# Optimization experiments

Hardware: AMD Instinct MI355X
Metric: run time of the kernel (lower is better)

Reference implementation:

```python
import jax, jax.numpy as jnp
import numpy as np

LN_EPS = 1e-5

def _ln(x, w, b):
    mu = jnp.mean(x, -1, keepdims=True)
    var = jnp.mean((x - mu) ** 2, -1, keepdims=True)
    return (x - mu) / jnp.sqrt(var + LN_EPS) * w + b

def _rot_fwd(x, c, s):
    dh = x.shape[-1] // 2
    r, i = x[..., :dh], x[..., dh:]
    return jnp.concatenate([r * c - i * s, r * s + i * c], axis=-1)

def _rot_inv(x, c, s):
    dh = x.shape[-1] // 2
    r, i = x[..., :dh], x[..., dh:]
    return jnp.concatenate([r * c + i * s, -r * s + i * c], axis=-1)

def _sheaf(x, thetas, alpha, corr_W):
    # causal offsets for window=3
    B, T, d = x.shape
    offsets = [-3, -2, -1, 0]
    lap = jnp.zeros_like(x)
    for idx, delta in enumerate(offsets):
        th = thetas[idx]
        c, s = jnp.cos(th), jnp.sin(th)
        Rx = _rot_fwd(x, c, s)
        if delta == 0:
            x_nb = x
        else:
            ad = -delta
            zeros = jnp.zeros((B, ad, d), dtype=x.dtype)
            x_nb = jnp.concatenate([zeros, x[:, :T - ad, :]], axis=1)
        lap = lap + _rot_inv(Rx - x_nb, c, s)
    out = x - jnp.abs(alpha) * lap
    return out + jnp.einsum('btd,od->bto', out, corr_W)

def _gist_rotation(x, gist_theta, gist_mag, gist_weights, gist_strength, ln_w, ln_b):
    # Scale-1 path: gist_weights present. theta: (B, dh)
    dh = x.shape[-1] // 2
    w = gist_weights[..., None] * gist_mag              # (B, K, 1)
    w = w / (jnp.sum(w, axis=1, keepdims=True) + 1e-8)
    theta = jnp.sum(w * gist_theta, axis=1)             # (B, dh)
    theta = theta * jax.nn.sigmoid(gist_strength)
    c = jnp.cos(theta)[:, None, :]                      # (B, 1, dh)
    s = jnp.sin(theta)[:, None, :]
    r, i = x[..., :dh], x[..., dh:]
    rot = jnp.concatenate([r * c - i * s, r * s + i * c], axis=-1)
    return _ln(rot, ln_w, ln_b)

def _gist_cross_attn(x, gist_theta, gist_mag, Wq, Wk, Wv, Wo, gist_up_W, gist_up_b, n_heads=16):
    B, T, d = x.shape
    K = gist_theta.shape[1]
    dh = d // n_heads
    gist_repr = jnp.einsum('bkf,of->bko', jnp.concatenate([gist_theta, gist_mag], axis=-1), gist_up_W) + gist_up_b  # (B,K,d)
    Q = jnp.einsum('btd,od->bto', x, Wq).reshape(B, T, n_heads, dh).transpose(0, 2, 1, 3)          # (B,H,T,dh)
    Kh = jnp.einsum('bkd,od->bko', gist_repr, Wk).reshape(B, K, n_heads, dh).transpose(0, 2, 1, 3)  # (B,H,K,dh)
    V = jnp.einsum('bkd,od->bko', gist_repr, Wv).reshape(B, K, n_heads, dh).transpose(0, 2, 1, 3)
    scores = jnp.einsum('bhtd,bhkd->bhtk', Q, Kh) / jnp.sqrt(jnp.asarray(dh, x.dtype))
    ctx = jnp.einsum('bhtk,bhkd->bhtd', jax.nn.softmax(scores, axis=-1), V)
    ctx = ctx.transpose(0, 2, 1, 3).reshape(B, T, d)
    return jnp.einsum('btd,od->bto', ctx, Wo)

def _forward(x, gist_theta, gist_mag, gist_weights,
             ln_sheaf_w, ln_sheaf_b, sheaf_thetas, alpha, corr_W,
             ln_gist_w, ln_gist_b, gist_strength, gr_ln_w, gr_ln_b,
             ln_gca_w, ln_gca_b, Wq, Wk, Wv, Wo, gist_up_W, gist_up_b):
    x = x + _sheaf(_ln(x, ln_sheaf_w, ln_sheaf_b), sheaf_thetas, alpha, corr_W)
    xn = _ln(x, ln_gist_w, ln_gist_b)
    x = x + (_gist_rotation(xn, gist_theta, gist_mag, gist_weights, gist_strength, gr_ln_w, gr_ln_b) - xn)
    x = x + _gist_cross_attn(_ln(x, ln_gca_w, ln_gca_b), gist_theta, gist_mag,
                             Wq, Wk, Wv, Wo, gist_up_W, gist_up_b)
    return x

def setup_inputs() -> dict:
    key = jax.random.key(0)
    ks = jax.random.split(key, 16)
    B, T, d, K = 4, 2048, 2048, 16
    dh = d // 2
    scale = 1.0 / np.sqrt(d)
    inp = {
        'x': jax.random.normal(ks[0], (B, T, d), jnp.float32),
        'gist_theta': jax.random.normal(ks[1], (B, K, dh), jnp.float32),
        'gist_mag': jax.random.uniform(ks[2], (B, K, 1), jnp.float32),
        'gist_weights': jax.random.uniform(ks[3], (B, K), jnp.float32),
        'ln_sheaf_w': jnp.ones((d,), jnp.float32),
        'ln_sheaf_b': jnp.zeros((d,), jnp.float32),
        'sheaf_thetas': 0.1 * jax.random.normal(ks[4], (4, dh), jnp.float32),
        'alpha': jnp.asarray(0.15, jnp.float32),
        'corr_W': scale * jax.random.normal(ks[5], (d, d), jnp.float32),
        'ln_gist_w': jnp.ones((d,), jnp.float32),
        'ln_gist_b': jnp.zeros((d,), jnp.float32),
        'gist_strength': jnp.asarray(0.0, jnp.float32),
        'gr_ln_w': jnp.ones((d,), jnp.float32),
        'gr_ln_b': jnp.zeros((d,), jnp.float32),
        'ln_gca_w': jnp.ones((d,), jnp.float32),
        'ln_gca_b': jnp.zeros((d,), jnp.float32),
        'Wq': scale * jax.random.normal(ks[6], (d, d), jnp.float32),
        'Wk': scale * jax.random.normal(ks[7], (d, d), jnp.float32),
        'Wv': scale * jax.random.normal(ks[8], (d, d), jnp.float32),
        'Wo': scale * jax.random.normal(ks[9], (d, d), jnp.float32),
        'gist_up_W': (1.0 / np.sqrt(dh + 1)) * jax.random.normal(ks[10], (d, dh + 1), jnp.float32),
        'gist_up_b': jnp.zeros((d,), jnp.float32),
    }
    return inp

def reference(x, gist_theta, gist_mag, gist_weights,
              ln_sheaf_w, ln_sheaf_b, sheaf_thetas, alpha, corr_W,
              ln_gist_w, ln_gist_b, gist_strength, gr_ln_w, gr_ln_b,
              ln_gca_w, ln_gca_b, Wq, Wk, Wv, Wo, gist_up_W, gist_up_b):
    return _forward(x, gist_theta, gist_mag, gist_weights,
                    ln_sheaf_w, ln_sheaf_b, sheaf_thetas, alpha, corr_W,
                    ln_gist_w, ln_gist_b, gist_strength, gr_ln_w, gr_ln_b,
                    ln_gca_w, ln_gca_b, Wq, Wk, Wv, Wo, gist_up_W, gist_up_b)
```

## Files before the change

kernel.cpp:

```cpp
#include <hip/hip_runtime.h>
#include <hip/hip_bf16.h>

typedef unsigned short u16;
typedef unsigned int   u32;

using frag_ab = __attribute__((ext_vector_type(8))) short;
using frag_cd = __attribute__((ext_vector_type(4))) float;

__device__ __forceinline__ float bf2f(u16 u) {
    union { u32 i; float f; } v; v.i = ((u32)u) << 16; return v.f;
}
__device__ __forceinline__ u16 f2bf(float f) {
    __hip_bfloat16 h = __float2bfloat16(f);
    u16 u; __builtin_memcpy(&u, &h, 2); return u;
}
__device__ __forceinline__ float lo2f(u32 u) { union { u32 i; float f; } v; v.i = u << 16; return v.f; }
__device__ __forceinline__ float hi2f(u32 u) { union { u32 i; float f; } v; v.i = u & 0xffff0000u; return v.f; }
__device__ __forceinline__ void unpack8(uint4 v, float* f) {
    f[0]=lo2f(v.x); f[1]=hi2f(v.x); f[2]=lo2f(v.y); f[3]=hi2f(v.y);
    f[4]=lo2f(v.z); f[5]=hi2f(v.z); f[6]=lo2f(v.w); f[7]=hi2f(v.w);
}
__device__ __forceinline__ void load4f(const u16* p, float* f) {
    ushort4 v = *reinterpret_cast<const ushort4*>(p);
    f[0]=bf2f(v.x); f[1]=bf2f(v.y); f[2]=bf2f(v.z); f[3]=bf2f(v.w);
}
__device__ __forceinline__ void store4bf(u16* p, const float* f) {
    ushort4 v; v.x=f2bf(f[0]); v.y=f2bf(f[1]); v.z=f2bf(f[2]); v.w=f2bf(f[3]);
    *reinterpret_cast<ushort4*>(p) = v;
}
__device__ __forceinline__ u32 pack2(float a, float b) {
    return (u32)f2bf(a) | ((u32)f2bf(b) << 16);
}

__device__ __forceinline__ void gld16(const u16* g, u16* l) {
    __builtin_amdgcn_global_load_lds(
        (const __attribute__((address_space(1))) u32*)g,
        (__attribute__((address_space(3))) u32*)l, 16, 0, 0);
}

__device__ __forceinline__ void block_reduce2(float& s, float& ss, float* red) {
    #pragma unroll
    for (int off = 32; off > 0; off >>= 1) {
        s  += __shfl_down(s, off, 64);
        ss += __shfl_down(ss, off, 64);
    }
    int wv = threadIdx.x >> 6, ln = threadIdx.x & 63;
    if (ln == 0) { red[wv*2] = s; red[wv*2+1] = ss; }
    __syncthreads();
    s  = red[0] + red[2] + red[4] + red[6];
    ss = red[1] + red[3] + red[5] + red[7];
    __syncthreads();
}

__global__ __launch_bounds__(256) void convert_kernel(
    const float* __restrict__ in, u16* __restrict__ out, int n4)
{
    int i = blockIdx.x * 256 + threadIdx.x;
    if (i < n4) {
        float4 v = reinterpret_cast<const float4*>(in)[i];
        ushort4 o; o.x=f2bf(v.x); o.y=f2bf(v.y); o.z=f2bf(v.z); o.w=f2bf(v.w);
        reinterpret_cast<ushort4*>(out)[i] = o;
    }
}

__global__ __launch_bounds__(256) void apad_kernel(
    const float* __restrict__ gth, const float* __restrict__ gmag,
    u16* __restrict__ Abuf)
{
    const int r = blockIdx.x;
    const int tid = threadIdx.x;
    for (int c0 = tid*4; c0 < 1056; c0 += 1024) {
        float f[4];
        #pragma unroll
        for (int i = 0; i < 4; ++i) {
            int c = c0 + i;
            f[i] = (c < 1024) ? gth[(size_t)r*1024 + c] : (c == 1024 ? gmag[r] : 0.f);
        }
        store4bf(Abuf + (size_t)r*1056 + c0, f);
    }
}

__global__ __launch_bounds__(256) void wpad_kernel(
    const float* __restrict__ upW, u16* __restrict__ Bbuf)
{
    const int r = blockIdx.x;
    const int tid = threadIdx.x;
    for (int c0 = tid*4; c0 < 1056; c0 += 1024) {
        float f[4];
        #pragma unroll
        for (int i = 0; i < 4; ++i) {
            int c = c0 + i;
            f[i] = (c < 1025) ? upW[(size_t)r*1025 + c] : 0.f;
        }
        store4bf(Bbuf + (size_t)r*1056 + c0, f);
    }
}

__global__ __launch_bounds__(256) void setup_kernel(
    const float* __restrict__ sheaf_th, const float* __restrict__ gth,
    const float* __restrict__ gmag, const float* __restrict__ gwts,
    const float* __restrict__ strength, float* __restrict__ sheaf_cs,
    float* __restrict__ gist_cs)
{
    int bx = blockIdx.x, tid = threadIdx.x;
    if (bx < 4) {
        for (int j = tid; j < 1024; j += 256) {
            float th = sheaf_th[bx*1024 + j];
            sheaf_cs[bx*1024 + j]        = cosf(th);
            sheaf_cs[4096 + bx*1024 + j] = sinf(th);
        }
    } else {
        int b = bx - 4;
        float w[16], wsum = 0.f;
        #pragma unroll
        for (int k = 0; k < 16; ++k) {
            w[k] = gwts[b*16+k] * gmag[b*16+k];
            wsum += w[k];
        }
        float inv = 1.f / (wsum + 1e-8f);
        float sig = 1.f / (1.f + expf(-strength[0]));
        for (int j = tid; j < 1024; j += 256) {
            float th = 0.f;
            #pragma unroll
            for (int k = 0; k < 16; ++k)
                th += w[k] * inv * gth[(size_t)(b*16+k)*1024 + j];
            th *= sig;
            gist_cs[b*1024 + j]        = cosf(th);
            gist_cs[4096 + b*1024 + j] = sinf(th);
        }
    }
}

__global__ __launch_bounds__(256) void ln_kernel(
    const float* __restrict__ in, const float* __restrict__ w,
    const float* __restrict__ b, u16* __restrict__ out)
{
    __shared__ float red[8];
    const size_t base = (size_t)blockIdx.x * 2048;
    const int e0 = threadIdx.x * 8;
    float x[8];
    *reinterpret_cast<float4*>(&x[0]) = *reinterpret_cast<const float4*>(in + base + e0);
    *reinterpret_cast<float4*>(&x[4]) = *reinterpret_cast<const float4*>(in + base + e0 + 4);
    float s = 0.f, ss = 0.f;
    #pragma unroll
    for (int i = 0; i < 8; ++i) { s += x[i]; ss += x[i]*x[i]; }
    block_reduce2(s, ss, red);
    const float mu = s * (1.f/2048.f);
    const float rin = rsqrtf(ss * (1.f/2048.f) - mu*mu + 1e-5f);
    float wv[8], bv[8];
    *reinterpret_cast<float4*>(&wv[0]) = *reinterpret_cast<const float4*>(w + e0);
    *reinterpret_cast<float4*>(&wv[4]) = *reinterpret_cast<const float4*>(w + e0 + 4);
    *reinterpret_cast<float4*>(&bv[0]) = *reinterpret_cast<const float4*>(b + e0);
    *reinterpret_cast<float4*>(&bv[4]) = *reinterpret_cast<const float4*>(b + e0 + 4);
    float o[8];
    #pragma unroll
    for (int i = 0; i < 8; ++i) o[i] = (x[i]-mu)*rin*wv[i] + bv[i];
    uint4 st = { pack2(o[0],o[1]), pack2(o[2],o[3]), pack2(o[4],o[5]), pack2(o[6],o[7]) };
    *reinterpret_cast<uint4*>(out + base + e0) = st;
}

__global__ __launch_bounds__(256) void sheaf_kernel(
    const u16* __restrict__ x1, const float* __restrict__ scs,
    const float* __restrict__ alpha_p, u16* __restrict__ pre)
{
    const int row = blockIdx.x;
    const int t = row & 2047;
    const int j0 = threadIdx.x * 4;
    const size_t base = (size_t)row * 2048;
    const float a = fabsf(alpha_p[0]);

    float xr[4], xi[4];
    load4f(x1 + base + j0, xr);
    load4f(x1 + base + 1024 + j0, xi);
    float lr[4], li[4];
    #pragma unroll
    for (int m = 0; m < 4; ++m) { lr[m] = 4.f*xr[m]; li[m] = 4.f*xi[m]; }

    #pragma unroll
    for (int idx = 0; idx < 4; ++idx) {
        const int sh = 3 - idx;
        if (t >= sh) {
            const float4 c4 = *reinterpret_cast<const float4*>(&scs[idx*1024 + j0]);
            const float4 s4 = *reinterpret_cast<const float4*>(&scs[4096 + idx*1024 + j0]);
            float c[4] = {c4.x, c4.y, c4.z, c4.w};
            float sn[4] = {s4.x, s4.y, s4.z, s4.w};
            float yr[4], yi[4];
            load4f(x1 + base - (size_t)sh*2048 + j0, yr);
            load4f(x1 + base - (size_t)sh*2048 + 1024 + j0, yi);
            #pragma unroll
            for (int m = 0; m < 4; ++m) {
                lr[m] -= yr[m]*c[m] + yi[m]*sn[m];
                li[m] -= yi[m]*c[m] - yr[m]*sn[m];
            }
        }
    }
    float pr[4], pi[4];
    #pragma unroll
    for (int m = 0; m < 4; ++m) { pr[m] = xr[m] - a*lr[m]; pi[m] = xi[m] - a*li[m]; }
    store4bf(pre + base + j0, pr);
    store4bf(pre + base + 1024 + j0, pi);
}

__global__ __launch_bounds__(256) void stage2_kernel(
    const u16* __restrict__ xA, const float* __restrict__ gcs,
    const float* __restrict__ lgw, const float* __restrict__ lgb,
    const float* __restrict__ grw, const float* __restrict__ grb,
    const float* __restrict__ gcaw, const float* __restrict__ gcab,
    u16* __restrict__ xB, u16* __restrict__ x2)
{
    __shared__ float red[8];
    const int row = blockIdx.x;
    const int b = row >> 11;
    const int j0 = threadIdx.x * 4;
    const size_t base = (size_t)row * 2048;

    float ar[4], ai[4];
    load4f(xA + base + j0, ar);
    load4f(xA + base + 1024 + j0, ai);

    float s = 0.f, ss = 0.f;
    #pragma unroll
    for (int m = 0; m < 4; ++m) { s += ar[m]+ai[m]; ss += ar[m]*ar[m] + ai[m]*ai[m]; }
    block_reduce2(s, ss, red);
    float mu = s * (1.f/2048.f);
    float rin = rsqrtf(ss * (1.f/2048.f) - mu*mu + 1e-5f);

    float w0[4], b0[4], w1[4], b1[4];
    *reinterpret_cast<float4*>(w0) = *reinterpret_cast<const float4*>(lgw + j0);
    *reinterpret_cast<float4*>(b0) = *reinterpret_cast<const float4*>(lgb + j0);
    *reinterpret_cast<float4*>(w1) = *reinterpret_cast<const float4*>(lgw + 1024 + j0);
    *reinterpret_cast<float4*>(b1) = *reinterpret_cast<const float4*>(lgb + 1024 + j0);
    float xnr[4], xni[4];
    #pragma unroll
    for (int m = 0; m < 4; ++m) {
        xnr[m] = (ar[m]-mu)*rin*w0[m] + b0[m];
        xni[m] = (ai[m]-mu)*rin*w1[m] + b1[m];
    }

    const float4 c4 = *reinterpret_cast<const float4*>(&gcs[b*1024 + j0]);
    const float4 s4 = *reinterpret_cast<const float4*>(&gcs[4096 + b*1024 + j0]);
    float c[4] = {c4.x, c4.y, c4.z, c4.w};
    float sn[4] = {s4.x, s4.y, s4.z, s4.w};
    float rr[4], ri[4];
    #pragma unroll
    for (int m = 0; m < 4; ++m) {
        rr[m] = xnr[m]*c[m] - xni[m]*sn[m];
        ri[m] = xnr[m]*sn[m] + xni[m]*c[m];
    }

    s = 0.f; ss = 0.f;
    #pragma unroll
    for (int m = 0; m < 4; ++m) { s += rr[m]+ri[m]; ss += rr[m]*rr[m] + ri[m]*ri[m]; }
    block_reduce2(s, ss, red);
    float mu2 = s * (1.f/2048.f);
    float rin2 = rsqrtf(ss * (1.f/2048.f) - mu2*mu2 + 1e-5f);

    *reinterpret_cast<float4*>(w0) = *reinterpret_cast<const float4*>(grw + j0);
    *reinterpret_cast<float4*>(b0) = *reinterpret_cast<const float4*>(grb + j0);
    *reinterpret_cast<float4*>(w1) = *reinterpret_cast<const float4*>(grw + 1024 + j0);
    *reinterpret_cast<float4*>(b1) = *reinterpret_cast<const float4*>(grb + 1024 + j0);
    float br[4], bi[4];
    #pragma unroll
    for (int m = 0; m < 4; ++m) {
        float gr_ = (rr[m]-mu2)*rin2*w0[m] + b0[m];
        float gi_ = (ri[m]-mu2)*rin2*w1[m] + b1[m];
        br[m] = ar[m] - xnr[m] + gr_;
        bi[m] = ai[m] - xni[m] + gi_;
    }
    store4bf(xB + base + j0, br);
    store4bf(xB + base + 1024 + j0, bi);

    s = 0.f; ss = 0.f;
    #pragma unroll
    for (int m = 0; m < 4; ++m) { s += br[m]+bi[m]; ss += br[m]*br[m] + bi[m]*bi[m]; }
    block_reduce2(s, ss, red);
    float mu3 = s * (1.f/2048.f);
    float rin3 = rsqrtf(ss * (1.f/2048.f) - mu3*mu3 + 1e-5f);

    *reinterpret_cast<float4*>(w0) = *reinterpret_cast<const float4*>(gcaw + j0);
    *reinterpret_cast<float4*>(b0) = *reinterpret_cast<const float4*>(gcab + j0);
    *reinterpret_cast<float4*>(w1) = *reinterpret_cast<const float4*>(gcaw + 1024 + j0);
    *reinterpret_cast<float4*>(b1) = *reinterpret_cast<const float4*>(gcab + 1024 + j0);
    float o0[4], o1[4];
    #pragma unroll
    for (int m = 0; m < 4; ++m) {
        o0[m] = (br[m]-mu3)*rin3*w0[m] + b0[m];
        o1[m] = (bi[m]-mu3)*rin3*w1[m] + b1[m];
    }
    store4bf(x2 + base + j0, o0);
    store4bf(x2 + base + 1024 + j0, o1);
}

__global__ __launch_bounds__(256) void attn_kernel(
    const u16* __restrict__ Q, const u16* __restrict__ KV,
    u16* __restrict__ ctx)
{
    const int wv = threadIdx.x >> 6;
    const int lane = threadIdx.x & 63;
    const int tg = blockIdx.x * 4 + wv;
    const int b = tg >> 11;
    const size_t base = (size_t)tg * 2048 + lane * 32;

    float q[32];
    #pragma unroll
    for (int c = 0; c < 4; ++c)
        unpack8(*reinterpret_cast<const uint4*>(Q + base + c*8), &q[c*8]);

    float sc[16];
    #pragma unroll
    for (int k = 0; k < 16; ++k) {
        const u16* kr = KV + (size_t)(b*16 + k) * 4096 + lane*32;
        float p = 0.f;
        #pragma unroll
        for (int c = 0; c < 4; ++c) {
            float kv8[8]; unpack8(*reinterpret_cast<const uint4*>(kr + c*8), kv8);
            #pragma unroll
            for (int e = 0; e < 8; ++e) p += q[c*8+e] * kv8[e];
        }
        sc[k] = p;
    }
    #pragma unroll
    for (int k = 0; k < 16; ++k) {
        sc[k] += __shfl_xor(sc[k], 1, 64);
        sc[k] += __shfl_xor(sc[k], 2, 64);
        sc[k] *= 0.08838834764831845f;
    }
    float m = sc[0];
    #pragma unroll
    for (int k = 1; k < 16; ++k) m = fmaxf(m, sc[k]);
    float sum = 0.f;
    #pragma unroll
    for (int k = 0; k < 16; ++k) { sc[k] = expf(sc[k]-m); sum += sc[k]; }
    const float inv = 1.f / sum;

    float o[32];
    #pragma unroll
    for (int e = 0; e < 32; ++e) o[e] = 0.f;
    #pragma unroll
    for (int k = 0; k < 16; ++k) {
        const float p = sc[k] * inv;
        const u16* vr = KV + (size_t)(b*16 + k) * 4096 + 2048 + lane*32;
        #pragma unroll
        for (int c = 0; c < 4; ++c) {
            float v8[8]; unpack8(*reinterpret_cast<const uint4*>(vr + c*8), v8);
            #pragma unroll
            for (int e = 0; e < 8; ++e) o[c*8+e] += p * v8[e];
        }
    }
    #pragma unroll
    for (int c = 0; c < 4; ++c) {
        uint4 st = { pack2(o[c*8+0],o[c*8+1]), pack2(o[c*8+2],o[c*8+3]),
                     pack2(o[c*8+4],o[c*8+5]), pack2(o[c*8+6],o[c*8+7]) };
        *reinterpret_cast<uint4*>(ctx + base + c*8) = st;
    }
}

#define BM 128
#define BN 128
#define BK 32

template<int OUTF32>
__global__ __launch_bounds__(256) void gemm_bt_kernel(
    const u16* __restrict__ A, const u16* __restrict__ B,
    void* __restrict__ Cv, const float* __restrict__ addf,
    const u16* __restrict__ addb, const float* __restrict__ biasN,
    int M, int N, int K)
{
    __shared__ u16 As[2][8*512];
    __shared__ u16 Bs[2][8*512];

    const int tid = threadIdx.x;
    const int lane = tid & 63;
    const int wave = tid >> 6;
    const int wm = wave >> 1;
    const int wn = wave & 1;
    const int row0 = blockIdx.y * BM;
    const int col0 = blockIdx.x * BN;

    frag_cd acc[4][4] = {};

    const int srow   = lane >> 2;
    const int schunk = (lane & 3) ^ ((lane >> 3) & 3);
    const int scol   = schunk * 8;
    const int s0 = wave, s1 = wave + 4;

    int ra0 = row0 + s0*16 + srow; if (ra0 >= M) ra0 = M - 1;
    int ra1 = row0 + s1*16 + srow; if (ra1 >= M) ra1 = M - 1;
    const u16* gA0 = A + (size_t)ra0 * K + scol;
    const u16* gA1 = A + (size_t)ra1 * K + scol;
    const u16* gB0 = B + (size_t)(col0 + s0*16 + srow) * K + scol;
    const u16* gB1 = B + (size_t)(col0 + s1*16 + srow) * K + scol;

    const int fr = lane & 15;
    const int fq8 = lane >> 4;
    const int fslot = (4*fr + (fq8 ^ ((fr >> 1) & 3))) * 8;

    const int nt = K / BK;

    gld16(gA0, &As[0][s0*512]);
    gld16(gA1, &As[0][s1*512]);
    gld16(gB0, &Bs[0][s0*512]);
    gld16(gB1, &Bs[0][s1*512]);
    __syncthreads();

    int cur = 0;
    for (int t = 0; t < nt; ++t) {
        if (t + 1 < nt) {
            const int kt = (t + 1) * BK;
            gld16(gA0 + kt, &As[cur^1][s0*512]);
            gld16(gA1 + kt, &As[cur^1][s1*512]);
            gld16(gB0 + kt, &Bs[cur^1][s0*512]);
            gld16(gB1 + kt, &Bs[cur^1][s1*512]);
        }

        frag_ab af[4], bf_[4];
        #pragma unroll
        for (int i = 0; i < 4; ++i)
            af[i] = *reinterpret_cast<const frag_ab*>(&As[cur][(wm*4 + i)*512 + fslot]);
        #pragma unroll
        for (int j = 0; j < 4; ++j)
            bf_[j] = *reinterpret_cast<const frag_ab*>(&Bs[cur][(wn*4 + j)*512 + fslot]);
        #pragma unroll
        for (int i = 0; i < 4; ++i)
            #pragma unroll
            for (int j = 0; j < 4; ++j)
                acc[i][j] = __builtin_amdgcn_mfma_f32_16x16x32_bf16(af[i], bf_[j], acc[i][j], 0, 0, 0);

        __syncthreads();
        cur ^= 1;
    }

    #pragma unroll
    for (int i = 0; i < 4; ++i) {
        #pragma unroll
        for (int j = 0; j < 4; ++j) {
            #pragma unroll
            for (int r = 0; r < 4; ++r) {
                const int grow = row0 + wm*64 + i*16 + (lane >> 4) * 4 + r;
                const int gcol = col0 + wn*64 + j*16 + (lane & 15);
                if (grow < M) {
                    const size_t idx = (size_t)grow * N + gcol;
                    float v = acc[i][j][r];
                    if (addf) v += addf[idx];
                    if (addb) v += bf2f(addb[idx]);
                    if (biasN) v += biasN[gcol];
                    if (OUTF32) reinterpret_cast<float*>(Cv)[idx] = v;
                    else        reinterpret_cast<u16*>(Cv)[idx] = f2bf(v);
                }
            }
        }
    }
}

template<int OUTF32>
__global__ __launch_bounds__(512, 2) void gemm256_kernel(
    const u16* __restrict__ A, const u16* __restrict__ B,
    void* __restrict__ Cv, const float* __restrict__ addf,
    const u16* __restrict__ addb, const float* __restrict__ biasN,
    int M, int N, int K)
{
    extern __shared__ u16 lds[];
    u16* Abase = lds;
    u16* Bbase = lds + 32768;

    const int tid  = threadIdx.x;
    const int lane = tid & 63;
    const int wave = tid >> 6;
    const int wm   = wave >> 2;
    const int wn   = wave & 3;
    const int row0 = blockIdx.y * 256;
    const int col0 = blockIdx.x * 256;

    const int srow = lane >> 2;
    const int scol = ((lane & 3) ^ ((lane >> 3) & 3)) * 8;

    const u16* pA = A + (size_t)(row0 + wave*16 + srow) * K + scol;
    const u16* pB = B + (size_t)(col0 + wave*16 + srow) * K + scol;
    const size_t h128 = (size_t)128 * K;

    const int ldsW = wave * 1024;

    const int fr = lane & 15;
    const int fq8 = lane >> 4;
    const int fslot = (4*fr + (fq8 ^ ((fr >> 1) & 3))) * 8;

    frag_cd acc[8][4] = {};
    frag_ab bfr[4][2];
    frag_ab afr[2][2][2];

#define STAGE256(SRC, DSTOFF, KT)                                   \
    gld16((SRC) + (KT),      (DSTOFF) + ldsW);                      \
    gld16((SRC) + (KT) + 32, (DSTOFF) + ldsW + 512);

    STAGE256(pB,        Bbase + 0*8192, 0);
    STAGE256(pB + h128, Bbase + 1*8192, 0);
    STAGE256(pA,        Abase + 0*8192, 0);
    STAGE256(pA + h128, Abase + 1*8192, 0);
    STAGE256(pB,        Bbase + 2*8192, 64);
    STAGE256(pB + h128, Bbase + 3*8192, 64);
    asm volatile("s_waitcnt vmcnt(4)" ::: "memory");
    __builtin_amdgcn_s_barrier();
    {
        const u16* Ah = Abase + (0*2 + wm)*8192;
        #pragma unroll
        for (int r = 0; r < 2; ++r)
            #pragma unroll
            for (int ks = 0; ks < 2; ++ks)
                afr[0][r][ks] = *reinterpret_cast<const frag_ab*>(
                    Ah + ((r)*2*1 + (2*0 + r)*0 + ((0 + r)*2 + ks)*512 - (r)*2 + fslot));
    }

    const int NI = K >> 7;
    for (int i = 0; i < NI; ++i) {
        const int t1k = i*128 + 64;
        int t2k = i*128 + 128; if (t2k >= K) t2k = K - 64;
        int t3k = i*128 + 192; if (t3k >= K) t3k = K - 64;

        #pragma unroll
        for (int p = 0; p < 8; ++p) {
            const int q = p & 3;
            const int bufc = p >> 2;

            if (q == 0) {
                const u16* Bh = Bbase + (bufc*2 + (wn >> 1))*8192;
                #pragma unroll
                for (int n = 0; n < 4; ++n)
                    #pragma unroll
                    for (int ks = 0; ks < 2; ++ks)
                        bfr[n][ks] = *reinterpret_cast<const frag_ab*>(
                            Bh + (((wn & 1)*4 + n)*2 + ks)*512 + fslot);
            }
            switch (p) {
                case 0: STAGE256(pA,        Abase + 2*8192, t1k); break;
                case 1: STAGE256(pA + h128, Abase + 3*8192, t1k); break;
                case 2: STAGE256(pB,        Bbase + 0*8192, t2k); break;
                case 3: STAGE256(pB + h128, Bbase + 1*8192, t2k); break;
                case 4: STAGE256(pA,        Abase + 0*8192, t2k); break;
                case 5: STAGE256(pA + h128, Abase + 1*8192, t2k); break;
                case 6: STAGE256(pB,        Bbase + 2*8192, t3k); break;
                case 7: STAGE256(pB + h128, Bbase + 3*8192, t3k); break;
            }
            if (q == 3) asm volatile("s_waitcnt vmcnt(4)" ::: "memory");
            __builtin_amdgcn_s_barrier();
            asm volatile("s_waitcnt lgkmcnt(0)" ::: "memory");
            __builtin_amdgcn_sched_barrier(0);

            {
                const int qn = (q + 1) & 3;
                const int bufn = (q == 3) ? (bufc ^ 1) : bufc;
                const u16* Ah = Abase + (bufn*2 + wm)*8192;
                #pragma unroll
                for (int r = 0; r < 2; ++r)
                    #pragma unroll
                    for (int ks = 0; ks < 2; ++ks)
                        afr[(p+1)&1][r][ks] = *reinterpret_cast<const frag_ab*>(
                            Ah + ((2*qn + r)*2 + ks)*512 + fslot);
            }

            __builtin_amdgcn_s_setprio(1);
            #pragma unroll
            for (int ks = 0; ks < 2; ++ks)
                #pragma unroll
                for (int r = 0; r < 2; ++r)
                    #pragma unroll
                    for (int n = 0; n < 4; ++n)
                        acc[2*q + r][n] = __builtin_amdgcn_mfma_f32_16x16x32_bf16(
                            afr[p&1][r][ks], bfr[n][ks], acc[2*q + r][n], 0, 0, 0);
            __builtin_amdgcn_s_setprio(0);
            __builtin_amdgcn_s_barrier();
        }
    }
    asm volatile("s_waitcnt vmcnt(0)" ::: "memory");
#undef STAGE256

    #pragma unroll
    for (int m = 0; m < 8; ++m) {
        #pragma unroll
        for (int n = 0; n < 4; ++n) {
            #pragma unroll
            for (int r = 0; r < 4; ++r) {
                const int grow = row0 + wm*128 + m*16 + (lane >> 4) * 4 + r;
                const int gcol = col0 + wn*64 + n*16 + (lane & 15);
                {
                    const size_t idx = (size_t)grow * N + gcol;
                    float v = acc[m][n][r];
                    if (addf) v += addf[idx];
                    if (addb) v += bf2f(addb[idx]);
                    if (biasN) v += biasN[gcol];
                    if (OUTF32) reinterpret_cast<float*>(Cv)[idx] = v;
                    else        reinterpret_cast<u16*>(Cv)[idx] = f2bf(v);
                }
            }
        }
    }
}

extern "C" void kernel_launch(void* const* d_in, const int* in_sizes, int n_in,
                              void* d_out, int out_size, void* d_ws, size_t ws_size,
                              hipStream_t stream)
{
    const float* x          = (const float*)d_in[0];
    const float* gist_theta = (const float*)d_in[1];
    const float* gist_mag   = (const float*)d_in[2];
    const float* gist_wts   = (const float*)d_in[3];
    const float* ln_sheaf_w = (const float*)d_in[4];
    const float* ln_sheaf_b = (const float*)d_in[5];
    const float* sheaf_th   = (const float*)d_in[6];
    const float* alpha      = (const float*)d_in[7];
    const float* corr_W     = (const float*)d_in[8];
    const float* ln_gist_w  = (const float*)d_in[9];
    const float* ln_gist_b  = (const float*)d_in[10];
    const float* strength   = (const float*)d_in[11];
    const float* gr_w       = (const float*)d_in[12];
    const float* gr_b       = (const float*)d_in[13];
    const float* gca_w      = (const float*)d_in[14];
    const float* gca_b      = (const float*)d_in[15];
    const float* Wq         = (const float*)d_in[16];
    const float* Wk         = (const float*)d_in[17];
    const float* Wv         = (const float*)d_in[18];
    const float* Wo         = (const float*)d_in[19];
    const float* up_W       = (const float*)d_in[20];
    const float* up_b       = (const float*)d_in[21];
    float* out = (float*)d_out;

    static bool attr_done = false;
    if (!attr_done) {
        hipFuncSetAttribute((const void*)&gemm256_kernel<0>,
                            hipFuncAttributeMaxDynamicSharedMemorySize, 131072);
        hipFuncSetAttribute((const void*)&gemm256_kernel<1>,
                            hipFuncAttributeMaxDynamicSharedMemorySize, 131072);
        attr_done = true;
    }

    char* w = (char*)d_ws;
    const size_t BIG = (size_t)4 * 2048 * 2048 * sizeof(u16);
    u16* wA = (u16*)(w);
    u16* wB = (u16*)(w + BIG);
    u16* wC = (u16*)(w + 2*BIG);
    u16* wslot = (u16*)(w + 3*BIG);
    char* small = w + 3*BIG + (size_t)2048*2048*sizeof(u16);
    float* sheaf_cs = (float*)(small);
    float* gist_cs  = (float*)(small + 32768);
    u16* repr = (u16*)(small + 65536);
    u16* KV   = repr + 64*2048;

    const int W4 = 2048*2048/4;
    const dim3 gBig256(2048/256, 8192/256), gKV(32, 1), gRepr(16, 1);

    setup_kernel<<<8, 256, 0, stream>>>(sheaf_th, gist_theta, gist_mag, gist_wts,
                                        strength, sheaf_cs, gist_cs);

    apad_kernel<<<64, 256, 0, stream>>>(gist_theta, gist_mag, wC);
    wpad_kernel<<<2048, 256, 0, stream>>>(up_W, wslot);
    gemm_bt_kernel<0><<<gRepr, 256, 0, stream>>>(wC, wslot, repr, nullptr, nullptr, up_b,
                                                 64, 2048, 1056);

    convert_kernel<<<4096, 256, 0, stream>>>(Wk, wB, W4);
    convert_kernel<<<4096, 256, 0, stream>>>(Wv, wB + (size_t)2048*2048, W4);
    gemm_bt_kernel<0><<<gKV, 256, 0, stream>>>(repr, wB, KV, nullptr, nullptr, nullptr,
                                               64, 4096, 2048);

    ln_kernel<<<8192, 256, 0, stream>>>(x, ln_sheaf_w, ln_sheaf_b, wA);
    sheaf_kernel<<<8192, 256, 0, stream>>>(wA, sheaf_cs, alpha, wB);

    convert_kernel<<<4096, 256, 0, stream>>>(corr_W, wslot, W4);
    gemm256_kernel<0><<<gBig256, 512, 131072, stream>>>(wB, wslot, wA, x, wB, nullptr,
                                                8192, 2048, 2048);
    stage2_kernel<<<8192, 256, 0, stream>>>(wA, gist_cs, ln_gist_w, ln_gist_b,
                                            gr_w, gr_b, gca_w, gca_b,
                                            wC, wA);
    convert_kernel<<<4096, 256, 0, stream>>>(Wq, wslot, W4);
    gemm256_kernel<0><<<gBig256, 512, 131072, stream>>>(wA, wslot, wB, nullptr, nullptr, nullptr,
                                                8192, 2048, 2048);
    attn_kernel<<<2048, 256, 0, stream>>>(wB, KV, wA);
    convert_kernel<<<4096, 256, 0, stream>>>(Wo, wslot, W4);
    gemm256_kernel<1><<<gBig256, 512, 131072, stream>>>(wA, wslot, (void*)out, nullptr, wC, nullptr,
                                                8192, 2048, 2048);
}
```

Before: 702.2 us.

## Split-K small gist GEMMs and restructure LDS fragment loads in big GEMM

Adds a split-K mode to the small 128x128 GEMM that writes per-slice fp32 partials, plus a reduction kernel that sums them, adds bias and converts to bf16. This is used for the M=64 repr and K/V projections, which previously launched only 16-32 blocks. Separately, the 256x256 GEMM now loads A fragments with inline ds_read_b128 within each phase instead of double-buffered register prefetch, with explicit lgkmcnt waits. The split path requires enough workspace and adds extra partial-buffer traffic and a launch; the GEMM change may reduce the overlap of LDS reads with MFMA work.

```diff
diff --git a/kernel.cpp b/kernel.cpp
--- a/kernel.cpp
+++ b/kernel.cpp
@@ -36,6 +36,16 @@
     __builtin_amdgcn_global_load_lds(
         (const __attribute__((address_space(1))) u32*)g,
         (__attribute__((address_space(3))) u32*)l, 16, 0, 0);
+}
+
+__device__ __forceinline__ u32 ldsaddr(const u16* p) {
+    return (u32)(uintptr_t)(const __attribute__((address_space(3))) u16*)p;
+}
+
+__device__ __forceinline__ frag_ab dsread16(u32 a) {
+    frag_ab r;
+    asm volatile("ds_read_b128 %0, %1" : "=v"(r) : "v"(a));
+    return r;
 }
 
 __device__ __forceinline__ void block_reduce2(float& s, float& ss, float* red) {
@@ -359,7 +369,7 @@
 #define BN 128
 #define BK 32
 
-template<int OUTF32>
+template<int OUTMODE>
 __global__ __launch_bounds__(256) void gemm_bt_kernel(
     const u16* __restrict__ A, const u16* __restrict__ B,
     void* __restrict__ Cv, const float* __restrict__ addf,
@@ -395,17 +405,22 @@
     const int fq8 = lane >> 4;
     const int fslot = (4*fr + (fq8 ^ ((fr >> 1) & 3))) * 8;
 
-    const int nt = K / BK;
-
-    gld16(gA0, &As[0][s0*512]);
-    gld16(gA1, &As[0][s1*512]);
-    gld16(gB0, &Bs[0][s0*512]);
-    gld16(gB1, &Bs[0][s1*512]);
+    const int nsteps = K / BK;
+    int ts = 0, te = nsteps;
+    if (OUTMODE == 2) {
+        ts = (nsteps * (int)blockIdx.z) / (int)gridDim.z;
+        te = (nsteps * ((int)blockIdx.z + 1)) / (int)gridDim.z;
+    }
+
+    gld16(gA0 + ts*BK, &As[0][s0*512]);
+    gld16(gA1 + ts*BK, &As[0][s1*512]);
+    gld16(gB0 + ts*BK, &Bs[0][s0*512]);
+    gld16(gB1 + ts*BK, &Bs[0][s1*512]);
     __syncthreads();
 
     int cur = 0;
-    for (int t = 0; t < nt; ++t) {
-        if (t + 1 < nt) {
+    for (int t = ts; t < te; ++t) {
+        if (t + 1 < te) {
             const int kt = (t + 1) * BK;
             gld16(gA0 + kt, &As[cur^1][s0*512]);
             gld16(gA1 + kt, &As[cur^1][s1*512]);
@@ -429,6 +444,9 @@
         __syncthreads();
         cur ^= 1;
     }
+
+    float* Pz = (OUTMODE == 2)
+        ? reinterpret_cast<float*>(Cv) + (size_t)blockIdx.z * M * N : nullptr;
 
     #pragma unroll
     for (int i = 0; i < 4; ++i) {
@@ -441,15 +459,39 @@
                 if (grow < M) {
                     const size_t idx = (size_t)grow * N + gcol;
                     float v = acc[i][j][r];
-                    if (addf) v += addf[idx];
-                    if (addb) v += bf2f(addb[idx]);
-                    if (biasN) v += biasN[gcol];
-                    if (OUTF32) reinterpret_cast<float*>(Cv)[idx] = v;
-                    else        reinterpret_cast<u16*>(Cv)[idx] = f2bf(v);
+                    if (OUTMODE == 2) {
+                        Pz[idx] = v;
+                    } else {
+                        if (addf) v += addf[idx];
+                        if (addb) v += bf2f(addb[idx]);
+                        if (biasN) v += biasN[gcol];
+                        if (OUTMODE == 1) reinterpret_cast<float*>(Cv)[idx] = v;
+                        else              reinterpret_cast<u16*>(Cv)[idx] = f2bf(v);
+                    }
                 }
             }
         }
     }
+}
+
+__global__ __launch_bounds__(256) void ksum_kernel(
+    const float* __restrict__ part, int nz, int n4, int N,
+    const float* __restrict__ biasN, u16* __restrict__ out)
+{
+    int i = blockIdx.x * 256 + threadIdx.x;
+    if (i >= n4) return;
+    const float4* p4 = reinterpret_cast<const float4*>(part);
+    float4 s = p4[i];
+    for (int z = 1; z < nz; ++z) {
+        float4 t = p4[i + (size_t)z * n4];
+        s.x += t.x; s.y += t.y; s.z += t.z; s.w += t.w;
+    }
+    if (biasN) {
+        int col = (i * 4) % N;
+        s.x += biasN[col]; s.y += biasN[col+1]; s.z += biasN[col+2]; s.w += biasN[col+3];
+    }
+    ushort4 o; o.x=f2bf(s.x); o.y=f2bf(s.y); o.z=f2bf(s.z); o.w=f2bf(s.w);
+    reinterpret_cast<ushort4*>(out)[i] = o;
 }
 
 template<int OUTF32>
@@ -482,11 +524,14 @@
 
     const int fr = lane & 15;
     const int fq8 = lane >> 4;
-    const int fslot = (4*fr + (fq8 ^ ((fr >> 1) & 3))) * 8;
+    const int fByte = (4*fr + (fq8 ^ ((fr >> 1) & 3))) * 16;
+
+    const u32 uA = ldsaddr(Abase) + (u32)(wm * 16384) + (u32)fByte;
+    const u32 uB = ldsaddr(Bbase) + (u32)((wn >> 1) * 16384 + (wn & 1) * 8192) + (u32)fByte;
 
     frag_cd acc[8][4] = {};
     frag_ab bfr[4][2];
-    frag_ab afr[2][2][2];
+    frag_ab afr[2][2];
 
 #define STAGE256(SRC, DSTOFF, KT)                                   \
     gld16((SRC) + (KT),      (DSTOFF) + ldsW);                      \
@@ -500,15 +545,6 @@
     STAGE256(pB + h128, Bbase + 3*8192, 64);
     asm volatile("s_waitcnt vmcnt(4)" ::: "memory");
     __builtin_amdgcn_s_barrier();
-    {
-        const u16* Ah = Abase + (0*2 + wm)*8192;
-        #pragma unroll
-        for (int r = 0; r < 2; ++r)
-            #pragma unroll
-            for (int ks = 0; ks < 2; ++ks)
-                afr[0][r][ks] = *reinterpret_cast<const frag_ab*>(
-                    Ah + ((r)*2*1 + (2*0 + r)*0 + ((0 + r)*2 + ks)*512 - (r)*2 + fslot));
-    }
 
     const int NI = K >> 7;
     for (int i = 0; i < NI; ++i) {
@@ -522,14 +558,18 @@
             const int bufc = p >> 2;
 
             if (q == 0) {
-                const u16* Bh = Bbase + (bufc*2 + (wn >> 1))*8192;
                 #pragma unroll
                 for (int n = 0; n < 4; ++n)
                     #pragma unroll
                     for (int ks = 0; ks < 2; ++ks)
-                        bfr[n][ks] = *reinterpret_cast<const frag_ab*>(
-                            Bh + (((wn & 1)*4 + n)*2 + ks)*512 + fslot);
+                        bfr[n][ks] = dsread16(uB + (u32)(bufc*32768 + (n*2 + ks)*1024));
             }
+            #pragma unroll
+            for (int r = 0; r < 2; ++r)
+                #pragma unroll
+                for (int ks = 0; ks < 2; ++ks)
+                    afr[r][ks] = dsread16(uA + (u32)(bufc*32768 + ((2*q + r)*2 + ks)*1024));
+
             switch (p) {
                 case 0: STAGE256(pA,        Abase + 2*8192, t1k); break;
                 case 1: STAGE256(pA + h128, Abase + 3*8192, t1k); break;
@@ -540,22 +580,11 @@
                 case 6: STAGE256(pB,        Bbase + 2*8192, t3k); break;
                 case 7: STAGE256(pB + h128, Bbase + 3*8192, t3k); break;
             }
+            if (q == 0) asm volatile("s_waitcnt lgkmcnt(8)" ::: "memory");
             if (q == 3) asm volatile("s_waitcnt vmcnt(4)" ::: "memory");
             __builtin_amdgcn_s_barrier();
             asm volatile("s_waitcnt lgkmcnt(0)" ::: "memory");
             __builtin_amdgcn_sched_barrier(0);
-
-            {
-                const int qn = (q + 1) & 3;
-                const int bufn = (q == 3) ? (bufc ^ 1) : bufc;
-                const u16* Ah = Abase + (bufn*2 + wm)*8192;
-                #pragma unroll
-                for (int r = 0; r < 2; ++r)
-                    #pragma unroll
-                    for (int ks = 0; ks < 2; ++ks)
-                        afr[(p+1)&1][r][ks] = *reinterpret_cast<const frag_ab*>(
-                            Ah + ((2*qn + r)*2 + ks)*512 + fslot);
-            }
 
             __builtin_amdgcn_s_setprio(1);
             #pragma unroll
@@ -565,7 +594,7 @@
                     #pragma unroll
                     for (int n = 0; n < 4; ++n)
                         acc[2*q + r][n] = __builtin_amdgcn_mfma_f32_16x16x32_bf16(
-                            afr[p&1][r][ks], bfr[n][ks], acc[2*q + r][n], 0, 0, 0);
+                            afr[r][ks], bfr[n][ks], acc[2*q + r][n], 0, 0, 0);
             __builtin_amdgcn_s_setprio(0);
             __builtin_amdgcn_s_barrier();
         }
@@ -581,15 +610,13 @@
             for (int r = 0; r < 4; ++r) {
                 const int grow = row0 + wm*128 + m*16 + (lane >> 4) * 4 + r;
                 const int gcol = col0 + wn*64 + n*16 + (lane & 15);
-                {
-                    const size_t idx = (size_t)grow * N + gcol;
-                    float v = acc[m][n][r];
-                    if (addf) v += addf[idx];
-                    if (addb) v += bf2f(addb[idx]);
-                    if (biasN) v += biasN[gcol];
-                    if (OUTF32) reinterpret_cast<float*>(Cv)[idx] = v;
-                    else        reinterpret_cast<u16*>(Cv)[idx] = f2bf(v);
-                }
+                const size_t idx = (size_t)grow * N + gcol;
+                float v = acc[m][n][r];
+                if (addf) v += addf[idx];
+                if (addb) v += bf2f(addb[idx]);
+                if (biasN) v += biasN[gcol];
+                if (OUTF32) reinterpret_cast<float*>(Cv)[idx] = v;
+                else        reinterpret_cast<u16*>(Cv)[idx] = f2bf(v);
             }
         }
     }
@@ -643,6 +670,9 @@
     float* gist_cs  = (float*)(small + 32768);
     u16* repr = (u16*)(small + 65536);
     u16* KV   = repr + 64*2048;
+    float* part = (float*)((char*)KV + (size_t)64*4096*sizeof(u16));
+    const size_t part_bytes = (size_t)8 * 64 * 4096 * sizeof(float);
+    const bool ksplit = ws_size >= (size_t)((char*)part - w) + part_bytes;
 
     const int W4 = 2048*2048/4;
     const dim3 gBig256(2048/256, 8192/256), gKV(32, 1), gRepr(16, 1);
@@ -652,13 +682,27 @@
 
     apad_kernel<<<64, 256, 0, stream>>>(gist_theta, gist_mag, wC);
     wpad_kernel<<<2048, 256, 0, stream>>>(up_W, wslot);
-    gemm_bt_kernel<0><<<gRepr, 256, 0, stream>>>(wC, wslot, repr, nullptr, nullptr, up_b,
-                                                 64, 2048, 1056);
+    if (ksplit) {
+        gemm_bt_kernel<2><<<dim3(16,1,4), 256, 0, stream>>>(wC, wslot, part,
+                                                 nullptr, nullptr, nullptr, 64, 2048, 1056);
+        ksum_kernel<<<(64*2048/4 + 255)/256, 256, 0, stream>>>(part, 4, 64*2048/4, 2048,
+                                                 up_b, repr);
+    } else {
+        gemm_bt_kernel<0><<<gRepr, 256, 0, stream>>>(wC, wslot, repr, nullptr, nullptr, up_b,
+                                                     64, 2048, 1056);
+    }
 
     convert_kernel<<<4096, 256, 0, stream>>>(Wk, wB, W4);
     convert_kernel<<<4096, 256, 0, stream>>>(Wv, wB + (size_t)2048*2048, W4);
-    gemm_bt_kernel<0><<<gKV, 256, 0, stream>>>(repr, wB, KV, nullptr, nullptr, nullptr,
-                                               64, 4096, 2048);
+    if (ksplit) {
+        gemm_bt_kernel<2><<<dim3(32,1,8), 256, 0, stream>>>(repr, wB, part,
+                                                 nullptr, nullptr, nullptr, 64, 4096, 2048);
+        ksum_kernel<<<(64*4096/4 + 255)/256, 256, 0, stream>>>(part, 8, 64*4096/4, 4096,
+                                                 nullptr, KV);
+    } else {
+        gemm_bt_kernel<0><<<gKV, 256, 0, stream>>>(repr, wB, KV, nullptr, nullptr, nullptr,
+                                                   64, 4096, 2048);
+    }
 
     ln_kernel<<<8192, 256, 0, stream>>>(x, ln_sheaf_w, ln_sheaf_b, wA);
     sheaf_kernel<<<8192, 256, 0, stream>>>(wA, sheaf_cs, alpha, wB);
```

Measured after the change: 647.2 us. 7.8% less time.
